# Optimization experiments

Measured on AMD Instinct MI355X. Metric: run time of the kernel, lower is better.

Reference implementation:

```python
import jax, jax.numpy as jnp
import numpy as np

N = 50000      # nodes
E = 800000     # directed edges (avg degree 16)
F_IN = 128     # in_channels
HID = 256      # hidden_channels
OUT = 40       # out_channels (classes)


def setup_inputs() -> dict:
    key = jax.random.key(0)
    ks = jax.random.split(key, 6)
    x = jax.random.normal(ks[0], (N, F_IN), dtype=jnp.float32)
    edge_index = jax.random.randint(ks[1], (2, E), 0, N, dtype=jnp.int32)
    W1 = jax.random.normal(ks[2], (F_IN, HID), dtype=jnp.float32) * (1.0 / np.sqrt(F_IN))
    b1 = jnp.zeros((HID,), jnp.float32)
    W2 = jax.random.normal(ks[3], (HID, HID), dtype=jnp.float32) * (1.0 / np.sqrt(HID))
    b2 = jnp.zeros((HID,), jnp.float32)
    Wc = jax.random.normal(ks[4], (HID, OUT), dtype=jnp.float32) * (1.0 / np.sqrt(HID))
    bc = jnp.zeros((OUT,), jnp.float32)
    return {"x": x, "W1": W1, "b1": b1, "W2": W2, "b2": b2,
            "Wc": Wc, "bc": bc, "edge_index": edge_index}


def _gcn_conv(x, W, b, src, dst, norm):
    # PyG GCNConv: linear transform, then normalized sparse aggregation, then bias.
    h = x @ W                                    # [N, H]
    msg = h[src] * norm[:, None]                 # [E+N, H] gather + scale
    agg = jax.ops.segment_sum(msg, dst, num_segments=N)  # scatter-add
    return agg + b


def reference(x, W1, b1, W2, b2, Wc, bc, edge_index):
    # add self-loops (GCNConv default add_self_loops=True)
    loops = jnp.arange(N, dtype=edge_index.dtype)
    src = jnp.concatenate([edge_index[0], loops])
    dst = jnp.concatenate([edge_index[1], loops])
    # symmetric normalization D^-1/2 A D^-1/2 (degree counted at dst)
    deg = jax.ops.segment_sum(jnp.ones_like(dst, dtype=jnp.float32), dst,
                              num_segments=N)
    dinv = jax.lax.rsqrt(jnp.maximum(deg, 1.0))  # deg >= 1 due to self-loops
    norm = dinv[src] * dinv[dst]                 # [E+N]
    # layer 1 + ReLU (dropout is identity in eval mode)
    h = jax.nn.relu(_gcn_conv(x, W1, b1, src, dst, norm))
    # layer 2 + ReLU
    h = jax.nn.relu(_gcn_conv(h, W2, b2, src, dst, norm))
    # dense classifier
    return h @ Wc + bc  # [N, OUT]
```

## Files before the change

### kernel.cpp

```cpp
#include <hip/hip_runtime.h>

#define NNODES 50000
#define NEDGES 800000
#define F_IN   128
#define HID    256
#define NOUT   40
#define NOUT_PAD 128
#define NBLK_SCAN ((NNODES + 255) / 256)

typedef __attribute__((ext_vector_type(8))) _Float16 f16x8;
typedef __attribute__((ext_vector_type(4))) float f32x4;

__device__ __forceinline__ unsigned short f2h(float f) {
  return __builtin_bit_cast(unsigned short, (_Float16)f);
}
__device__ __forceinline__ float h2f(unsigned short u) {
  return (float)__builtin_bit_cast(_Float16, u);
}


__global__ __launch_bounds__(256) void k_degree(const int* __restrict__ dst,
                                                int* __restrict__ count) {
  int e = blockIdx.x * 256 + threadIdx.x;
  if (e < NEDGES) atomicAdd(&count[dst[e]], 1);
}

__global__ __launch_bounds__(256) void k_scan1(const int* __restrict__ count,
                                               int* __restrict__ rowstart,
                                               int* __restrict__ bsum,
                                               float* __restrict__ dinv) {
  __shared__ int tmp[256];
  int t = threadIdx.x;
  int i = blockIdx.x * 256 + t;
  int v = (i < NNODES) ? count[i] : 0;
  if (i < NNODES) dinv[i] = rsqrtf((float)(v + 1));
  tmp[t] = v;
  __syncthreads();
  for (int off = 1; off < 256; off <<= 1) {
    int x = (t >= off) ? tmp[t - off] : 0;
    __syncthreads();
    tmp[t] += x;
    __syncthreads();
  }
  if (i < NNODES) rowstart[i] = tmp[t] - v;
  if (t == 255) bsum[blockIdx.x] = tmp[255];
}

__global__ __launch_bounds__(256) void k_scan2(const int* __restrict__ bsum,
                                               int* __restrict__ boff) {
  __shared__ int tmp[256];
  int t = threadIdx.x;
  int v = (t < NBLK_SCAN) ? bsum[t] : 0;
  tmp[t] = v;
  __syncthreads();
  for (int off = 1; off < 256; off <<= 1) {
    int x = (t >= off) ? tmp[t - off] : 0;
    __syncthreads();
    tmp[t] += x;
    __syncthreads();
  }
  if (t < NBLK_SCAN) boff[t] = tmp[t] - v;
}

__global__ __launch_bounds__(256) void k_scan3(int* __restrict__ rowstart,
                                               const int* __restrict__ boff) {
  int i = blockIdx.x * 256 + threadIdx.x;
  if (i < NNODES) rowstart[i] += boff[blockIdx.x];
  if (i == 0) rowstart[NNODES] = NEDGES;
}

__global__ __launch_bounds__(256) void k_scatter(const int* __restrict__ src,
                                                 const int* __restrict__ dst,
                                                 const int* __restrict__ rowstart,
                                                 int* __restrict__ cursor,
                                                 int* __restrict__ csr) {
  int e = blockIdx.x * 256 + threadIdx.x;
  if (e >= NEDGES) return;
  int d = dst[e];
  int p = rowstart[d] + atomicAdd(&cursor[d], 1);
  csr[p] = src[e];
}


__global__ __launch_bounds__(256) void k_cast(const float* __restrict__ X,
                                              unsigned short* __restrict__ Xh) {
  int i = blockIdx.x * 256 + threadIdx.x;
  if (i * 4 >= NNODES * F_IN) return;
  float4 v = *reinterpret_cast<const float4*>(X + (size_t)i * 4);
  ushort4 o;
  o.x = f2h(v.x); o.y = f2h(v.y); o.z = f2h(v.z); o.w = f2h(v.w);
  *reinterpret_cast<ushort4*>(Xh + (size_t)i * 4) = o;
}


__global__ __launch_bounds__(256) void k_prep(const float* __restrict__ W, int K, int N,
                                              int Nvalid, int Npad,
                                              unsigned short* __restrict__ T) {
  int idx = blockIdx.x * 256 + threadIdx.x;
  if (idx >= Npad * K) return;
  int n = idx / K, k = idx - n * K;
  float v = (n < Nvalid) ? W[(size_t)k * N + n] : 0.f;
  T[idx] = f2h(v);
}


__global__ __launch_bounds__(256) void k_agg1(const unsigned short* __restrict__ X,
                                              const int* __restrict__ rowstart,
                                              const int* __restrict__ csr,
                                              const float* __restrict__ dinv,
                                              unsigned int* __restrict__ Y) {
  int wave = threadIdx.x >> 6, lane = threadIdx.x & 63;
  int node = blockIdx.x * 4 + wave;
  if (node >= NNODES) return;
  float di = dinv[node];
  float a0, a1;
  {
    ushort2 v = *reinterpret_cast<const ushort2*>(X + (size_t)node * F_IN + lane * 2);
    a0 = h2f(v.x) * di * di; a1 = h2f(v.y) * di * di;
  }
  int e = rowstart[node], end = rowstart[node + 1];
  for (; e + 4 <= end; e += 4) {
    int s0 = csr[e], s1 = csr[e + 1], s2 = csr[e + 2], s3 = csr[e + 3];
    float w0 = dinv[s0] * di, w1 = dinv[s1] * di;
    float w2 = dinv[s2] * di, w3 = dinv[s3] * di;
    ushort2 r0 = *reinterpret_cast<const ushort2*>(X + (size_t)s0 * F_IN + lane * 2);
    ushort2 r1 = *reinterpret_cast<const ushort2*>(X + (size_t)s1 * F_IN + lane * 2);
    ushort2 r2 = *reinterpret_cast<const ushort2*>(X + (size_t)s2 * F_IN + lane * 2);
    ushort2 r3 = *reinterpret_cast<const ushort2*>(X + (size_t)s3 * F_IN + lane * 2);
    a0 = fmaf(h2f(r0.x), w0, a0); a1 = fmaf(h2f(r0.y), w0, a1);
    a0 = fmaf(h2f(r1.x), w1, a0); a1 = fmaf(h2f(r1.y), w1, a1);
    a0 = fmaf(h2f(r2.x), w2, a0); a1 = fmaf(h2f(r2.y), w2, a1);
    a0 = fmaf(h2f(r3.x), w3, a0); a1 = fmaf(h2f(r3.y), w3, a1);
  }
  for (; e < end; ++e) {
    int s = csr[e];
    float w = dinv[s] * di;
    ushort2 r = *reinterpret_cast<const ushort2*>(X + (size_t)s * F_IN + lane * 2);
    a0 = fmaf(h2f(r.x), w, a0); a1 = fmaf(h2f(r.y), w, a1);
  }
  Y[(size_t)node * 64 + lane] = (unsigned)f2h(a0) | ((unsigned)f2h(a1) << 16);
}


__global__ __launch_bounds__(256) void k_agg2(const unsigned short* __restrict__ H,
                                              const int* __restrict__ rowstart,
                                              const int* __restrict__ csr,
                                              const float* __restrict__ dinv,
                                              uint2* __restrict__ Y) {
  int wave = threadIdx.x >> 6, lane = threadIdx.x & 63;
  int node = blockIdx.x * 4 + wave;
  if (node >= NNODES) return;
  float di = dinv[node];
  float a0, a1, a2, a3;
  {
    ushort4 v = *reinterpret_cast<const ushort4*>(H + (size_t)node * HID + lane * 4);
    a0 = h2f(v.x) * di * di; a1 = h2f(v.y) * di * di;
    a2 = h2f(v.z) * di * di; a3 = h2f(v.w) * di * di;
  }
  int e = rowstart[node], end = rowstart[node + 1];
  for (; e + 4 <= end; e += 4) {
    int s0 = csr[e], s1 = csr[e + 1], s2 = csr[e + 2], s3 = csr[e + 3];
    float w0 = dinv[s0] * di, w1 = dinv[s1] * di;
    float w2 = dinv[s2] * di, w3 = dinv[s3] * di;
    ushort4 r0 = *reinterpret_cast<const ushort4*>(H + (size_t)s0 * HID + lane * 4);
    ushort4 r1 = *reinterpret_cast<const ushort4*>(H + (size_t)s1 * HID + lane * 4);
    ushort4 r2 = *reinterpret_cast<const ushort4*>(H + (size_t)s2 * HID + lane * 4);
    ushort4 r3 = *reinterpret_cast<const ushort4*>(H + (size_t)s3 * HID + lane * 4);
    a0 = fmaf(h2f(r0.x), w0, a0); a1 = fmaf(h2f(r0.y), w0, a1);
    a2 = fmaf(h2f(r0.z), w0, a2); a3 = fmaf(h2f(r0.w), w0, a3);
    a0 = fmaf(h2f(r1.x), w1, a0); a1 = fmaf(h2f(r1.y), w1, a1);
    a2 = fmaf(h2f(r1.z), w1, a2); a3 = fmaf(h2f(r1.w), w1, a3);
    a0 = fmaf(h2f(r2.x), w2, a0); a1 = fmaf(h2f(r2.y), w2, a1);
    a2 = fmaf(h2f(r2.z), w2, a2); a3 = fmaf(h2f(r2.w), w2, a3);
    a0 = fmaf(h2f(r3.x), w3, a0); a1 = fmaf(h2f(r3.y), w3, a1);
    a2 = fmaf(h2f(r3.z), w3, a2); a3 = fmaf(h2f(r3.w), w3, a3);
  }
  for (; e < end; ++e) {
    int s = csr[e];
    float w = dinv[s] * di;
    ushort4 r = *reinterpret_cast<const ushort4*>(H + (size_t)s * HID + lane * 4);
    a0 = fmaf(h2f(r.x), w, a0); a1 = fmaf(h2f(r.y), w, a1);
    a2 = fmaf(h2f(r.z), w, a2); a3 = fmaf(h2f(r.w), w, a3);
  }
  uint2 o;
  o.x = (unsigned)f2h(a0) | ((unsigned)f2h(a1) << 16);
  o.y = (unsigned)f2h(a2) | ((unsigned)f2h(a3) << 16);
  Y[(size_t)node * 64 + lane] = o;
}


template <int RELU, int OMODE>
__global__ __launch_bounds__(256) void k_mgemm(const unsigned short* __restrict__ Ag,
                                               const unsigned short* __restrict__ Btg,
                                               const float* __restrict__ bias,
                                               void* __restrict__ Cout,
                                               int M, int Nc, int K) {
  __shared__ unsigned short Ah[128 * 40], Bh[128 * 40];
  int tid = threadIdx.x;
  int lane = tid & 63, w = tid >> 6;
  int wr = w >> 1, wc = w & 1;
  int bm = blockIdx.x * 128, bn = blockIdx.y * 128;
  int l15 = lane & 15, kg = lane >> 4;

  f32x4 zero = {0.f, 0.f, 0.f, 0.f};
  f32x4 acc[4][4];
#pragma unroll
  for (int i = 0; i < 4; i++)
#pragma unroll
    for (int j = 0; j < 4; j++) acc[i][j] = zero;

  for (int kt = 0; kt < K; kt += 32) {
#pragma unroll
    for (int it = 0; it < 2; it++) {
      int c = tid + it * 256;
      int row = c >> 2, kq = c & 3;
      int ldso = row * 40 + kq * 8;
      {
        int gm = bm + row;
        uint4 v = {0, 0, 0, 0};
        if (gm < M) v = *reinterpret_cast<const uint4*>(Ag + (size_t)gm * K + kt + kq * 8);
        *reinterpret_cast<uint4*>(&Ah[ldso]) = v;
      }
      {
        size_t g = (size_t)(bn + row) * K + kt + kq * 8;
        *reinterpret_cast<uint4*>(&Bh[ldso]) = *reinterpret_cast<const uint4*>(Btg + g);
      }
    }
    __syncthreads();

    f16x8 fa[4], fb[4];
#pragma unroll
    for (int f = 0; f < 4; f++) {
      int ra = (wr * 64 + f * 16 + l15) * 40 + kg * 8;
      fa[f] = *reinterpret_cast<const f16x8*>(&Ah[ra]);
      int rb = (wc * 64 + f * 16 + l15) * 40 + kg * 8;
      fb[f] = *reinterpret_cast<const f16x8*>(&Bh[rb]);
    }
#pragma unroll
    for (int i = 0; i < 4; i++)
#pragma unroll
      for (int j = 0; j < 4; j++)
        acc[i][j] = __builtin_amdgcn_mfma_f32_16x16x32_f16(fa[i], fb[j], acc[i][j], 0, 0, 0);
    __syncthreads();
  }

  int r0 = kg * 4;
#pragma unroll
  for (int i = 0; i < 4; i++) {
    int gmBase = bm + wr * 64 + i * 16 + r0;
#pragma unroll
    for (int r = 0; r < 4; r++) {
      int gm = gmBase + r;
      if (gm >= M) continue;
#pragma unroll
      for (int j = 0; j < 4; j++) {
        int gn = bn + wc * 64 + j * 16 + l15;
        if (gn >= Nc) continue;
        float v = acc[i][j][r] + bias[gn];
        if (RELU) v = fmaxf(v, 0.f);
        size_t o = (size_t)gm * Nc + gn;
        if (OMODE == 0) ((float*)Cout)[o] = v;
        else            ((unsigned short*)Cout)[o] = f2h(v);
      }
    }
  }
}


extern "C" void kernel_launch(void* const* d_in, const int* in_sizes, int n_in,
                              void* d_out, int out_size, void* d_ws, size_t ws_size,
                              hipStream_t stream) {
  (void)in_sizes; (void)n_in; (void)out_size; (void)ws_size;
  const float* x  = (const float*)d_in[0];
  const float* W1 = (const float*)d_in[1];
  const float* b1 = (const float*)d_in[2];
  const float* W2 = (const float*)d_in[3];
  const float* b2 = (const float*)d_in[4];
  const float* Wc = (const float*)d_in[5];
  const float* bc = (const float*)d_in[6];
  const int* edge = (const int*)d_in[7];
  const int* srcE = edge;
  const int* dstE = edge + NEDGES;
  float* out = (float*)d_out;

  char* ws = (char*)d_ws;
  int*   count    = (int*)(ws + 0);
  int*   cursor   = (int*)(ws + 200064);
  int*   rowstart = (int*)(ws + 400128);
  float* dinv     = (float*)(ws + 600320);
  int*   csr      = (int*)(ws + 800384);
  int*   bsum     = (int*)(ws + 4000512);
  int*   boff     = (int*)(ws + 4001536);
  unsigned short* W1t = (unsigned short*)(ws + 4002560);
  unsigned short* W2t = (unsigned short*)(ws + 4068096);
  unsigned short* Wct = (unsigned short*)(ws + 4199168);
  unsigned short* xh  = (unsigned short*)(ws + 4264704);
  unsigned short* aggx = (unsigned short*)(ws + 17064704);
  unsigned short* h1   = (unsigned short*)(ws + 29864704);
  unsigned short* aggh = (unsigned short*)(ws + 55464704);
  unsigned short* h2   = (unsigned short*)(ws + 81064704);

  hipMemsetAsync(ws, 0, 400128, stream);

  k_cast<<<(NNODES * F_IN / 4 + 255) / 256, 256, 0, stream>>>(x, xh);
  k_degree<<<(NEDGES + 255) / 256, 256, 0, stream>>>(dstE, count);
  k_scan1<<<NBLK_SCAN, 256, 0, stream>>>(count, rowstart, bsum, dinv);
  k_scan2<<<1, 256, 0, stream>>>(bsum, boff);
  k_scan3<<<NBLK_SCAN, 256, 0, stream>>>(rowstart, boff);
  k_scatter<<<(NEDGES + 255) / 256, 256, 0, stream>>>(srcE, dstE, rowstart, cursor, csr);

  k_prep<<<(HID * F_IN + 255) / 256, 256, 0, stream>>>(W1, F_IN, HID, HID, HID, W1t);
  k_prep<<<(HID * HID + 255) / 256, 256, 0, stream>>>(W2, HID, HID, HID, HID, W2t);
  k_prep<<<(NOUT_PAD * HID + 255) / 256, 256, 0, stream>>>(Wc, HID, NOUT, NOUT, NOUT_PAD, Wct);

  k_agg1<<<(NNODES + 3) / 4, 256, 0, stream>>>(xh, rowstart, csr, dinv, (unsigned int*)aggx);
  {
    dim3 grid((NNODES + 127) / 128, HID / 128);
    k_mgemm<1, 1><<<grid, 256, 0, stream>>>(aggx, W1t, b1, (void*)h1, NNODES, HID, F_IN);
  }
  k_agg2<<<(NNODES + 3) / 4, 256, 0, stream>>>(h1, rowstart, csr, dinv, (uint2*)aggh);
  {
    dim3 grid((NNODES + 127) / 128, HID / 128);
    k_mgemm<1, 1><<<grid, 256, 0, stream>>>(aggh, W2t, b2, (void*)h2, NNODES, HID, HID);
  }
  {
    dim3 grid((NNODES + 127) / 128, NOUT_PAD / 128);
    k_mgemm<0, 0><<<grid, 256, 0, stream>>>(h2, Wct, bc, (void*)out, NNODES, NOUT, HID);
  }
}
```

Baseline: 366.2 us.

## Fuse prep kernels, split-wave edge aggregation, double-buffer GEMM, dedicated classifier

Merges the cast and degree kernels, and the three weight-transpose kernels, into single launches to cut launch overhead. The aggregation kernels now have each half-wave process alternate edges with wider vector loads, then combine the halves with a cross-lane shuffle; this doubles the number of neighbor rows in flight per wave. The MFMA GEMM gains register-staged double-buffered shared-memory tiles so the next K-tile's global loads overlap compute. The classifier gets its own kernel padded to 48 output columns instead of 128, which removes wasted MFMA work, at the cost of more code and higher LDS use.

```diff
diff --git a/kernel.cpp b/kernel.cpp
--- a/kernel.cpp
+++ b/kernel.cpp
@@ -5,11 +5,15 @@
 #define F_IN   128
 #define HID    256
 #define NOUT   40
-#define NOUT_PAD 128
+#define NOUT_PAD 48
 #define NBLK_SCAN ((NNODES + 255) / 256)
+#define NBLK_CAST 6250
+#define NBLK_DEG  3125
 
 typedef __attribute__((ext_vector_type(8))) _Float16 f16x8;
 typedef __attribute__((ext_vector_type(4))) float f32x4;
+typedef __attribute__((ext_vector_type(4))) unsigned short u16x4;
+typedef __attribute__((ext_vector_type(8))) unsigned short u16x8;
 
 __device__ __forceinline__ unsigned short f2h(float f) {
   return __builtin_bit_cast(unsigned short, (_Float16)f);
@@ -19,11 +23,22 @@
 }
 
 
-__global__ __launch_bounds__(256) void k_degree(const int* __restrict__ dst,
-                                                int* __restrict__ count) {
-  int e = blockIdx.x * 256 + threadIdx.x;
-  if (e < NEDGES) atomicAdd(&count[dst[e]], 1);
-}
+__global__ __launch_bounds__(256) void k_pre(const float* __restrict__ X,
+                                             unsigned short* __restrict__ Xh,
+                                             const int* __restrict__ dst,
+                                             int* __restrict__ count) {
+  if (blockIdx.x < NBLK_CAST) {
+    int i = blockIdx.x * 256 + threadIdx.x;
+    float4 v = *reinterpret_cast<const float4*>(X + (size_t)i * 4);
+    ushort4 o;
+    o.x = f2h(v.x); o.y = f2h(v.y); o.z = f2h(v.z); o.w = f2h(v.w);
+    *reinterpret_cast<ushort4*>(Xh + (size_t)i * 4) = o;
+  } else {
+    int e = (blockIdx.x - NBLK_CAST) * 256 + threadIdx.x;
+    if (e < NEDGES) atomicAdd(&count[dst[e]], 1);
+  }
+}
+
 
 __global__ __launch_bounds__(256) void k_scan1(const int* __restrict__ count,
                                                int* __restrict__ rowstart,
@@ -82,67 +97,31 @@
 }
 
 
-__global__ __launch_bounds__(256) void k_cast(const float* __restrict__ X,
-                                              unsigned short* __restrict__ Xh) {
-  int i = blockIdx.x * 256 + threadIdx.x;
-  if (i * 4 >= NNODES * F_IN) return;
-  float4 v = *reinterpret_cast<const float4*>(X + (size_t)i * 4);
-  ushort4 o;
-  o.x = f2h(v.x); o.y = f2h(v.y); o.z = f2h(v.z); o.w = f2h(v.w);
-  *reinterpret_cast<ushort4*>(Xh + (size_t)i * 4) = o;
-}
-
-
-__global__ __launch_bounds__(256) void k_prep(const float* __restrict__ W, int K, int N,
-                                              int Nvalid, int Npad,
-                                              unsigned short* __restrict__ T) {
-  int idx = blockIdx.x * 256 + threadIdx.x;
-  if (idx >= Npad * K) return;
-  int n = idx / K, k = idx - n * K;
-  float v = (n < Nvalid) ? W[(size_t)k * N + n] : 0.f;
-  T[idx] = f2h(v);
+__global__ __launch_bounds__(256) void k_prep3(const float* __restrict__ W1,
+                                               const float* __restrict__ W2,
+                                               const float* __restrict__ Wc,
+                                               unsigned short* __restrict__ T1,
+                                               unsigned short* __restrict__ T2,
+                                               unsigned short* __restrict__ Tc) {
+  int b = blockIdx.x;
+  if (b < 128) {
+    int idx = b * 256 + threadIdx.x;
+    int n = idx >> 7, k = idx & 127;
+    T1[idx] = f2h(W1[(size_t)k * HID + n]);
+  } else if (b < 384) {
+    int idx = (b - 128) * 256 + threadIdx.x;
+    int n = idx >> 8, k = idx & 255;
+    T2[idx] = f2h(W2[(size_t)k * HID + n]);
+  } else {
+    int idx = (b - 384) * 256 + threadIdx.x;
+    int n = idx >> 8, k = idx & 255;
+    float v = (n < NOUT) ? Wc[(size_t)k * NOUT + n] : 0.f;
+    Tc[idx] = f2h(v);
+  }
 }
 
 
 __global__ __launch_bounds__(256) void k_agg1(const unsigned short* __restrict__ X,
-                                              const int* __restrict__ rowstart,
-                                              const int* __restrict__ csr,
-                                              const float* __restrict__ dinv,
-                                              unsigned int* __restrict__ Y) {
-  int wave = threadIdx.x >> 6, lane = threadIdx.x & 63;
-  int node = blockIdx.x * 4 + wave;
-  if (node >= NNODES) return;
-  float di = dinv[node];
-  float a0, a1;
-  {
-    ushort2 v = *reinterpret_cast<const ushort2*>(X + (size_t)node * F_IN + lane * 2);
-    a0 = h2f(v.x) * di * di; a1 = h2f(v.y) * di * di;
-  }
-  int e = rowstart[node], end = rowstart[node + 1];
-  for (; e + 4 <= end; e += 4) {
-    int s0 = csr[e], s1 = csr[e + 1], s2 = csr[e + 2], s3 = csr[e + 3];
-    float w0 = dinv[s0] * di, w1 = dinv[s1] * di;
-    float w2 = dinv[s2] * di, w3 = dinv[s3] * di;
-    ushort2 r0 = *reinterpret_cast<const ushort2*>(X + (size_t)s0 * F_IN + lane * 2);
-    ushort2 r1 = *reinterpret_cast<const ushort2*>(X + (size_t)s1 * F_IN + lane * 2);
-    ushort2 r2 = *reinterpret_cast<const ushort2*>(X + (size_t)s2 * F_IN + lane * 2);
-    ushort2 r3 = *reinterpret_cast<const ushort2*>(X + (size_t)s3 * F_IN + lane * 2);
-    a0 = fmaf(h2f(r0.x), w0, a0); a1 = fmaf(h2f(r0.y), w0, a1);
-    a0 = fmaf(h2f(r1.x), w1, a0); a1 = fmaf(h2f(r1.y), w1, a1);
-    a0 = fmaf(h2f(r2.x), w2, a0); a1 = fmaf(h2f(r2.y), w2, a1);
-    a0 = fmaf(h2f(r3.x), w3, a0); a1 = fmaf(h2f(r3.y), w3, a1);
-  }
-  for (; e < end; ++e) {
-    int s = csr[e];
-    float w = dinv[s] * di;
-    ushort2 r = *reinterpret_cast<const ushort2*>(X + (size_t)s * F_IN + lane * 2);
-    a0 = fmaf(h2f(r.x), w, a0); a1 = fmaf(h2f(r.y), w, a1);
-  }
-  Y[(size_t)node * 64 + lane] = (unsigned)f2h(a0) | ((unsigned)f2h(a1) << 16);
-}
-
-
-__global__ __launch_bounds__(256) void k_agg2(const unsigned short* __restrict__ H,
                                               const int* __restrict__ rowstart,
                                               const int* __restrict__ csr,
                                               const float* __restrict__ dinv,
@@ -150,42 +129,113 @@
   int wave = threadIdx.x >> 6, lane = threadIdx.x & 63;
   int node = blockIdx.x * 4 + wave;
   if (node >= NNODES) return;
+  int half = lane >> 5, l32 = lane & 31;
   float di = dinv[node];
-  float a0, a1, a2, a3;
-  {
-    ushort4 v = *reinterpret_cast<const ushort4*>(H + (size_t)node * HID + lane * 4);
-    a0 = h2f(v.x) * di * di; a1 = h2f(v.y) * di * di;
-    a2 = h2f(v.z) * di * di; a3 = h2f(v.w) * di * di;
-  }
+  float a[4] = {0.f, 0.f, 0.f, 0.f};
   int e = rowstart[node], end = rowstart[node + 1];
-  for (; e + 4 <= end; e += 4) {
-    int s0 = csr[e], s1 = csr[e + 1], s2 = csr[e + 2], s3 = csr[e + 3];
+  for (; e + 8 <= end; e += 8) {
+    int s0 = csr[e + 0 + half], s1 = csr[e + 2 + half];
+    int s2 = csr[e + 4 + half], s3 = csr[e + 6 + half];
     float w0 = dinv[s0] * di, w1 = dinv[s1] * di;
     float w2 = dinv[s2] * di, w3 = dinv[s3] * di;
-    ushort4 r0 = *reinterpret_cast<const ushort4*>(H + (size_t)s0 * HID + lane * 4);
-    ushort4 r1 = *reinterpret_cast<const ushort4*>(H + (size_t)s1 * HID + lane * 4);
-    ushort4 r2 = *reinterpret_cast<const ushort4*>(H + (size_t)s2 * HID + lane * 4);
-    ushort4 r3 = *reinterpret_cast<const ushort4*>(H + (size_t)s3 * HID + lane * 4);
-    a0 = fmaf(h2f(r0.x), w0, a0); a1 = fmaf(h2f(r0.y), w0, a1);
-    a2 = fmaf(h2f(r0.z), w0, a2); a3 = fmaf(h2f(r0.w), w0, a3);
-    a0 = fmaf(h2f(r1.x), w1, a0); a1 = fmaf(h2f(r1.y), w1, a1);
-    a2 = fmaf(h2f(r1.z), w1, a2); a3 = fmaf(h2f(r1.w), w1, a3);
-    a0 = fmaf(h2f(r2.x), w2, a0); a1 = fmaf(h2f(r2.y), w2, a1);
-    a2 = fmaf(h2f(r2.z), w2, a2); a3 = fmaf(h2f(r2.w), w2, a3);
-    a0 = fmaf(h2f(r3.x), w3, a0); a1 = fmaf(h2f(r3.y), w3, a1);
-    a2 = fmaf(h2f(r3.z), w3, a2); a3 = fmaf(h2f(r3.w), w3, a3);
-  }
-  for (; e < end; ++e) {
+    u16x4 r0 = *reinterpret_cast<const u16x4*>(X + (size_t)s0 * F_IN + l32 * 4);
+    u16x4 r1 = *reinterpret_cast<const u16x4*>(X + (size_t)s1 * F_IN + l32 * 4);
+    u16x4 r2 = *reinterpret_cast<const u16x4*>(X + (size_t)s2 * F_IN + l32 * 4);
+    u16x4 r3 = *reinterpret_cast<const u16x4*>(X + (size_t)s3 * F_IN + l32 * 4);
+#pragma unroll
+    for (int k = 0; k < 4; k++) {
+      a[k] = fmaf(h2f(r0[k]), w0, a[k]);
+      a[k] = fmaf(h2f(r1[k]), w1, a[k]);
+      a[k] = fmaf(h2f(r2[k]), w2, a[k]);
+      a[k] = fmaf(h2f(r3[k]), w3, a[k]);
+    }
+  }
+  for (; e + 2 <= end; e += 2) {
+    int s = csr[e + half];
+    float w = dinv[s] * di;
+    u16x4 r = *reinterpret_cast<const u16x4*>(X + (size_t)s * F_IN + l32 * 4);
+#pragma unroll
+    for (int k = 0; k < 4; k++) a[k] = fmaf(h2f(r[k]), w, a[k]);
+  }
+  if (e < end) {
     int s = csr[e];
+    float w = half ? 0.f : dinv[s] * di;
+    u16x4 r = *reinterpret_cast<const u16x4*>(X + (size_t)s * F_IN + l32 * 4);
+#pragma unroll
+    for (int k = 0; k < 4; k++) a[k] = fmaf(h2f(r[k]), w, a[k]);
+  }
+#pragma unroll
+  for (int k = 0; k < 4; k++) a[k] += __shfl_xor(a[k], 32);
+  if (half == 0) {
+    u16x4 self = *reinterpret_cast<const u16x4*>(X + (size_t)node * F_IN + l32 * 4);
+    float dd = di * di;
+#pragma unroll
+    for (int k = 0; k < 4; k++) a[k] = fmaf(h2f(self[k]), dd, a[k]);
+    uint2 o;
+    o.x = (unsigned)f2h(a[0]) | ((unsigned)f2h(a[1]) << 16);
+    o.y = (unsigned)f2h(a[2]) | ((unsigned)f2h(a[3]) << 16);
+    Y[(size_t)node * 32 + l32] = o;
+  }
+}
+
+
+__global__ __launch_bounds__(256) void k_agg2(const unsigned short* __restrict__ H,
+                                              const int* __restrict__ rowstart,
+                                              const int* __restrict__ csr,
+                                              const float* __restrict__ dinv,
+                                              uint4* __restrict__ Y) {
+  int wave = threadIdx.x >> 6, lane = threadIdx.x & 63;
+  int node = blockIdx.x * 4 + wave;
+  if (node >= NNODES) return;
+  int half = lane >> 5, l32 = lane & 31;
+  float di = dinv[node];
+  float a[8] = {0.f, 0.f, 0.f, 0.f, 0.f, 0.f, 0.f, 0.f};
+  int e = rowstart[node], end = rowstart[node + 1];
+  for (; e + 8 <= end; e += 8) {
+    int s0 = csr[e + 0 + half], s1 = csr[e + 2 + half];
+    int s2 = csr[e + 4 + half], s3 = csr[e + 6 + half];
+    float w0 = dinv[s0] * di, w1 = dinv[s1] * di;
+    float w2 = dinv[s2] * di, w3 = dinv[s3] * di;
+    u16x8 r0 = *reinterpret_cast<const u16x8*>(H + (size_t)s0 * HID + l32 * 8);
+    u16x8 r1 = *reinterpret_cast<const u16x8*>(H + (size_t)s1 * HID + l32 * 8);
+    u16x8 r2 = *reinterpret_cast<const u16x8*>(H + (size_t)s2 * HID + l32 * 8);
+    u16x8 r3 = *reinterpret_cast<const u16x8*>(H + (size_t)s3 * HID + l32 * 8);
+#pragma unroll
+    for (int k = 0; k < 8; k++) {
+      a[k] = fmaf(h2f(r0[k]), w0, a[k]);
+      a[k] = fmaf(h2f(r1[k]), w1, a[k]);
+      a[k] = fmaf(h2f(r2[k]), w2, a[k]);
+      a[k] = fmaf(h2f(r3[k]), w3, a[k]);
+    }
+  }
+  for (; e + 2 <= end; e += 2) {
+    int s = csr[e + half];
     float w = dinv[s] * di;
-    ushort4 r = *reinterpret_cast<const ushort4*>(H + (size_t)s * HID + lane * 4);
-    a0 = fmaf(h2f(r.x), w, a0); a1 = fmaf(h2f(r.y), w, a1);
-    a2 = fmaf(h2f(r.z), w, a2); a3 = fmaf(h2f(r.w), w, a3);
-  }
-  uint2 o;
-  o.x = (unsigned)f2h(a0) | ((unsigned)f2h(a1) << 16);
-  o.y = (unsigned)f2h(a2) | ((unsigned)f2h(a3) << 16);
-  Y[(size_t)node * 64 + lane] = o;
+    u16x8 r = *reinterpret_cast<const u16x8*>(H + (size_t)s * HID + l32 * 8);
+#pragma unroll
+    for (int k = 0; k < 8; k++) a[k] = fmaf(h2f(r[k]), w, a[k]);
+  }
+  if (e < end) {
+    int s = csr[e];
+    float w = half ? 0.f : dinv[s] * di;
+    u16x8 r = *reinterpret_cast<const u16x8*>(H + (size_t)s * HID + l32 * 8);
+#pragma unroll
+    for (int k = 0; k < 8; k++) a[k] = fmaf(h2f(r[k]), w, a[k]);
+  }
+#pragma unroll
+  for (int k = 0; k < 8; k++) a[k] += __shfl_xor(a[k], 32);
+  if (half == 0) {
+    u16x8 self = *reinterpret_cast<const u16x8*>(H + (size_t)node * HID + l32 * 8);
+    float dd = di * di;
+#pragma unroll
+    for (int k = 0; k < 8; k++) a[k] = fmaf(h2f(self[k]), dd, a[k]);
+    uint4 o;
+    o.x = (unsigned)f2h(a[0]) | ((unsigned)f2h(a[1]) << 16);
+    o.y = (unsigned)f2h(a[2]) | ((unsigned)f2h(a[3]) << 16);
+    o.z = (unsigned)f2h(a[4]) | ((unsigned)f2h(a[5]) << 16);
+    o.w = (unsigned)f2h(a[6]) | ((unsigned)f2h(a[7]) << 16);
+    Y[(size_t)node * 32 + l32] = o;
+  }
 }
 
 
@@ -195,12 +245,15 @@
                                                const float* __restrict__ bias,
                                                void* __restrict__ Cout,
                                                int M, int Nc, int K) {
-  __shared__ unsigned short Ah[128 * 40], Bh[128 * 40];
+  __shared__ unsigned short Ah[2][128 * 40];
+  __shared__ unsigned short Bh[2][128 * 40];
   int tid = threadIdx.x;
   int lane = tid & 63, w = tid >> 6;
   int wr = w >> 1, wc = w & 1;
   int bm = blockIdx.x * 128, bn = blockIdx.y * 128;
   int l15 = lane & 15, kg = lane >> 4;
+  int row0 = tid >> 2, kq0 = (tid & 3) * 8;
+  int gm0 = bm + row0, gm1 = bm + row0 + 64;
 
   f32x4 zero = {0.f, 0.f, 0.f, 0.f};
   f32x4 acc[4][4];
@@ -209,40 +262,48 @@
 #pragma unroll
     for (int j = 0; j < 4; j++) acc[i][j] = zero;
 
-  for (int kt = 0; kt < K; kt += 32) {
-#pragma unroll
-    for (int it = 0; it < 2; it++) {
-      int c = tid + it * 256;
-      int row = c >> 2, kq = c & 3;
-      int ldso = row * 40 + kq * 8;
-      {
-        int gm = bm + row;
-        uint4 v = {0, 0, 0, 0};
-        if (gm < M) v = *reinterpret_cast<const uint4*>(Ag + (size_t)gm * K + kt + kq * 8);
-        *reinterpret_cast<uint4*>(&Ah[ldso]) = v;
-      }
-      {
-        size_t g = (size_t)(bn + row) * K + kt + kq * 8;
-        *reinterpret_cast<uint4*>(&Bh[ldso]) = *reinterpret_cast<const uint4*>(Btg + g);
-      }
-    }
-    __syncthreads();
-
+  uint4 ra0, ra1, rb0, rb1;
+  const uint4 z4 = {0, 0, 0, 0};
+#define LOADT(KT)                                                                    \
+  {                                                                                  \
+    ra0 = z4; ra1 = z4;                                                              \
+    if (gm0 < M) ra0 = *reinterpret_cast<const uint4*>(Ag + (size_t)gm0 * K + (KT) + kq0); \
+    if (gm1 < M) ra1 = *reinterpret_cast<const uint4*>(Ag + (size_t)gm1 * K + (KT) + kq0); \
+    rb0 = *reinterpret_cast<const uint4*>(Btg + (size_t)(bn + row0) * K + (KT) + kq0);     \
+    rb1 = *reinterpret_cast<const uint4*>(Btg + (size_t)(bn + row0 + 64) * K + (KT) + kq0);\
+  }
+#define STORET(B)                                                       \
+  {                                                                     \
+    *reinterpret_cast<uint4*>(&Ah[B][row0 * 40 + kq0]) = ra0;           \
+    *reinterpret_cast<uint4*>(&Ah[B][(row0 + 64) * 40 + kq0]) = ra1;    \
+    *reinterpret_cast<uint4*>(&Bh[B][row0 * 40 + kq0]) = rb0;           \
+    *reinterpret_cast<uint4*>(&Bh[B][(row0 + 64) * 40 + kq0]) = rb1;    \
+  }
+
+  LOADT(0);
+  STORET(0);
+  __syncthreads();
+  int nt = K >> 5, cur = 0;
+  for (int t = 0; t < nt; t++) {
+    bool pf = (t + 1 < nt);
+    if (pf) LOADT((t + 1) << 5);
     f16x8 fa[4], fb[4];
 #pragma unroll
     for (int f = 0; f < 4; f++) {
-      int ra = (wr * 64 + f * 16 + l15) * 40 + kg * 8;
-      fa[f] = *reinterpret_cast<const f16x8*>(&Ah[ra]);
-      int rb = (wc * 64 + f * 16 + l15) * 40 + kg * 8;
-      fb[f] = *reinterpret_cast<const f16x8*>(&Bh[rb]);
+      fa[f] = *reinterpret_cast<const f16x8*>(&Ah[cur][(wr * 64 + f * 16 + l15) * 40 + kg * 8]);
+      fb[f] = *reinterpret_cast<const f16x8*>(&Bh[cur][(wc * 64 + f * 16 + l15) * 40 + kg * 8]);
     }
 #pragma unroll
     for (int i = 0; i < 4; i++)
 #pragma unroll
       for (int j = 0; j < 4; j++)
         acc[i][j] = __builtin_amdgcn_mfma_f32_16x16x32_f16(fa[i], fb[j], acc[i][j], 0, 0, 0);
-    __syncthreads();
-  }
+    if (pf) STORET(cur ^ 1);
+    __syncthreads();
+    cur ^= 1;
+  }
+#undef LOADT
+#undef STORET
 
   int r0 = kg * 4;
 #pragma unroll
@@ -261,6 +322,74 @@
         size_t o = (size_t)gm * Nc + gn;
         if (OMODE == 0) ((float*)Cout)[o] = v;
         else            ((unsigned short*)Cout)[o] = f2h(v);
+      }
+    }
+  }
+}
+
+
+__global__ __launch_bounds__(256) void k_cls(const unsigned short* __restrict__ Ag,
+                                             const unsigned short* __restrict__ Btg,
+                                             const float* __restrict__ bias,
+                                             float* __restrict__ C, int M) {
+  __shared__ unsigned short As[256 * 40];
+  __shared__ unsigned short Bs[48 * 40];
+  int tid = threadIdx.x;
+  int lane = tid & 63, w = tid >> 6;
+  int l15 = lane & 15, kg = lane >> 4;
+  int bm = blockIdx.x * 256;
+
+  f32x4 zero = {0.f, 0.f, 0.f, 0.f};
+  f32x4 acc[4][3];
+#pragma unroll
+  for (int i = 0; i < 4; i++)
+#pragma unroll
+    for (int j = 0; j < 3; j++) acc[i][j] = zero;
+
+  for (int kt = 0; kt < HID; kt += 32) {
+#pragma unroll
+    for (int it = 0; it < 4; it++) {
+      int c = tid + it * 256;
+      int row = c >> 2, kq = (c & 3) * 8;
+      int gm = bm + row;
+      uint4 v = {0, 0, 0, 0};
+      if (gm < M) v = *reinterpret_cast<const uint4*>(Ag + (size_t)gm * HID + kt + kq);
+      *reinterpret_cast<uint4*>(&As[row * 40 + kq]) = v;
+    }
+    if (tid < 192) {
+      int row = tid >> 2, kq = (tid & 3) * 8;
+      *reinterpret_cast<uint4*>(&Bs[row * 40 + kq]) =
+          *reinterpret_cast<const uint4*>(Btg + (size_t)row * HID + kt + kq);
+    }
+    __syncthreads();
+    f16x8 fa[4], fb[3];
+#pragma unroll
+    for (int f = 0; f < 4; f++)
+      fa[f] = *reinterpret_cast<const f16x8*>(&As[(w * 64 + f * 16 + l15) * 40 + kg * 8]);
+#pragma unroll
+    for (int j = 0; j < 3; j++)
+      fb[j] = *reinterpret_cast<const f16x8*>(&Bs[(j * 16 + l15) * 40 + kg * 8]);
+#pragma unroll
+    for (int i = 0; i < 4; i++)
+#pragma unroll
+      for (int j = 0; j < 3; j++)
+        acc[i][j] = __builtin_amdgcn_mfma_f32_16x16x32_f16(fa[i], fb[j], acc[i][j], 0, 0, 0);
+    __syncthreads();
+  }
+
+  int r0 = kg * 4;
+#pragma unroll
+  for (int i = 0; i < 4; i++) {
+    int gmBase = bm + w * 64 + i * 16 + r0;
+#pragma unroll
+    for (int r = 0; r < 4; r++) {
+      int gm = gmBase + r;
+      if (gm >= M) continue;
+#pragma unroll
+      for (int j = 0; j < 3; j++) {
+        int gn = j * 16 + l15;
+        if (gn >= NOUT) continue;
+        C[(size_t)gm * NOUT + gn] = acc[i][j][r] + bias[gn];
       }
     }
   }
@@ -302,29 +431,22 @@
 
   hipMemsetAsync(ws, 0, 400128, stream);
 
-  k_cast<<<(NNODES * F_IN / 4 + 255) / 256, 256, 0, stream>>>(x, xh);
-  k_degree<<<(NEDGES + 255) / 256, 256, 0, stream>>>(dstE, count);
+  k_pre<<<NBLK_CAST + NBLK_DEG, 256, 0, stream>>>(x, xh, dstE, count);
   k_scan1<<<NBLK_SCAN, 256, 0, stream>>>(count, rowstart, bsum, dinv);
   k_scan2<<<1, 256, 0, stream>>>(bsum, boff);
   k_scan3<<<NBLK_SCAN, 256, 0, stream>>>(rowstart, boff);
   k_scatter<<<(NEDGES + 255) / 256, 256, 0, stream>>>(srcE, dstE, rowstart, cursor, csr);
-
-  k_prep<<<(HID * F_IN + 255) / 256, 256, 0, stream>>>(W1, F_IN, HID, HID, HID, W1t);
-  k_prep<<<(HID * HID + 255) / 256, 256, 0, stream>>>(W2, HID, HID, HID, HID, W2t);
-  k_prep<<<(NOUT_PAD * HID + 255) / 256, 256, 0, stream>>>(Wc, HID, NOUT, NOUT, NOUT_PAD, Wct);
-
-  k_agg1<<<(NNODES + 3) / 4, 256, 0, stream>>>(xh, rowstart, csr, dinv, (unsigned int*)aggx);
+  k_prep3<<<432, 256, 0, stream>>>(W1, W2, Wc, W1t, W2t, Wct);
+
+  k_agg1<<<(NNODES + 3) / 4, 256, 0, stream>>>(xh, rowstart, csr, dinv, (uint2*)aggx);
   {
     dim3 grid((NNODES + 127) / 128, HID / 128);
     k_mgemm<1, 1><<<grid, 256, 0, stream>>>(aggx, W1t, b1, (void*)h1, NNODES, HID, F_IN);
   }
-  k_agg2<<<(NNODES + 3) / 4, 256, 0, stream>>>(h1, rowstart, csr, dinv, (uint2*)aggh);
+  k_agg2<<<(NNODES + 3) / 4, 256, 0, stream>>>(h1, rowstart, csr, dinv, (uint4*)aggh);
   {
     dim3 grid((NNODES + 127) / 128, HID / 128);
     k_mgemm<1, 1><<<grid, 256, 0, stream>>>(aggh, W2t, b2, (void*)h2, NNODES, HID, HID);
   }
-  {
-    dim3 grid((NNODES + 127) / 128, NOUT_PAD / 128);
-    k_mgemm<0, 0><<<grid, 256, 0, stream>>>(h2, Wct, bc, (void*)out, NNODES, NOUT, HID);
-  }
-}
+  k_cls<<<(NNODES + 255) / 256, 256, 0, stream>>>(h2, Wct, bc, out, NNODES);
+}
```

Result: faster. 351.7 us (-4.0%).
